# Kernel optimization log

Measured on AMD Instinct MI355X. Metric: run time of the kernel, lower is better.

Reference implementation:

```python
import jax, jax.numpy as jnp
import numpy as np

D_MODEL = 1024
D_HIDDEN = 4096
BATCH = 4
SEQ = 2048
EPS = 1e-5
SLOPE = 0.01  # LeakyReLU default negative_slope


def layer_norm(x, g, b):
    m = jnp.mean(x, axis=-1, keepdims=True)
    v = jnp.mean(jnp.square(x - m), axis=-1, keepdims=True)
    return (x - m) * jax.lax.rsqrt(v + EPS) * g + b


def leaky_relu(x):
    return jnp.where(x >= 0, x, SLOPE * x)


def setup_inputs() -> dict:
    key = jax.random.key(0)
    ks = jax.random.split(key, 8)
    scale = D_MODEL ** 0.5
    x = jax.random.normal(ks[0], (BATCH, SEQ, D_MODEL), dtype=jnp.float32)
    qk = jax.random.normal(ks[1], (D_MODEL, D_MODEL), dtype=jnp.float32) / scale
    ov = jax.random.normal(ks[2], (D_MODEL, D_MODEL), dtype=jnp.float32) / scale
    ln1_g = jnp.ones((D_MODEL,), jnp.float32)
    ln1_b = jnp.zeros((D_MODEL,), jnp.float32)
    ln2_g = jnp.ones((D_MODEL,), jnp.float32)
    ln2_b = jnp.zeros((D_MODEL,), jnp.float32)
    # nn.Linear default init: uniform(-1/sqrt(fan_in), 1/sqrt(fan_in))
    def lin(k, fan_in, fan_out):
        k1, k2 = jax.random.split(k)
        bd = 1.0 / np.sqrt(fan_in)
        W = jax.random.uniform(k1, (fan_out, fan_in), jnp.float32, -bd, bd)
        b = jax.random.uniform(k2, (fan_out,), jnp.float32, -bd, bd)
        return W, b
    W_up, b_up = lin(ks[3], D_MODEL, D_HIDDEN)
    W_h, b_h = lin(ks[4], D_HIDDEN, D_HIDDEN)
    W_down, b_down = lin(ks[5], D_HIDDEN, D_MODEL)
    return {"x": x, "qk": qk, "ov": ov, "ln1_g": ln1_g, "ln1_b": ln1_b,
            "ln2_g": ln2_g, "ln2_b": ln2_b, "W_up": W_up, "b_up": b_up,
            "W_h": W_h, "b_h": b_h, "W_down": W_down, "b_down": b_down}


def reference(x, qk, ov, ln1_g, ln1_b, ln2_g, ln2_b,
              W_up, b_up, W_h, b_h, W_down, b_down):
    scale = D_MODEL ** 0.5
    # --- attention on ln1(x) ---
    h = layer_norm(x, ln1_g, ln1_b)                     # [B,S,D]
    scores = jnp.einsum('bsd,de,bte->bst', h, qk, h) / scale  # [B,S,S]
    n = h.shape[1]
    causal = jnp.tril(jnp.ones((n, n), bool))
    scores = jnp.where(causal, scores, -jnp.inf)
    probs = jax.nn.softmax(scores, axis=-1)
    attn = jnp.einsum('bst,btd,de->bse', probs, h, ov)  # [B,S,D]
    x = x + attn
    # --- MLP on ln2(x) ---
    h2 = layer_norm(x, ln2_g, ln2_b)
    a = leaky_relu(h2 @ W_up.T + b_up)
    a = leaky_relu(a @ W_h.T + b_h)
    a = leaky_relu(a @ W_down.T + b_down)
    return x + a
```

## Files before the change

kernel.cpp:

```cpp
#include <hip/hip_runtime.h>
#include <stdint.h>


typedef __attribute__((ext_vector_type(4))) float  f32x4;
typedef __attribute__((ext_vector_type(8))) __bf16 bf16v8;
typedef __attribute__((ext_vector_type(8))) unsigned short u16x8;
typedef unsigned short ushort_t;
typedef unsigned int   u32;

#define SLOPE 0.01f

__device__ __forceinline__ ushort_t f2bf(float f) {
  u32 u = __builtin_bit_cast(u32, f);
  u32 r = (u + 0x7FFFu + ((u >> 16) & 1u)) >> 16;
  return (ushort_t)r;
}
__device__ __forceinline__ float bf2f(ushort_t b) {
  u32 u = ((u32)b) << 16;
  return __builtin_bit_cast(float, u);
}

__device__ __forceinline__ void gload_lds16(const void* g, void* l) {
  __builtin_amdgcn_global_load_lds(
      (const __attribute__((address_space(1))) u32*)g,
      (__attribute__((address_space(3))) u32*)l, 16, 0, 0);
}

template<int EPI>
__global__ __launch_bounds__(512, 1)
void gemm_nt8(const ushort_t* __restrict__ A, const ushort_t* __restrict__ B,
              void* __restrict__ Cv, const float* __restrict__ bias,
              int M, int N, int K)
{
  extern __shared__ char smem[];
  const ushort_t* lds = (const ushort_t*)smem;
  const int tid = threadIdx.x;
  const int l   = tid & 63;
  const int m0 = blockIdx.y * 256;
  const int n0 = blockIdx.x * 256;
  const int wid = tid >> 6;
  const int wm = (wid >> 2) * 128;
  const int wn = (wid & 3) * 64;
  const int nt = K >> 5;

  const int  sg      = (((tid & 3) ^ ((tid >> 3) & 3))) * 8;
  const long rowA0   = (long)(m0 +       (tid >> 2)) * K;
  const long rowA1   = (long)(m0 + 128 + (tid >> 2)) * K;
  const long rowB0   = (long)(n0 +       (tid >> 2)) * K;
  const long rowB1   = (long)(n0 + 128 + (tid >> 2)) * K;
  const int  wbase16 = (tid & ~63) * 16;

#define STAGE(TT) do {                                                        \
    const long _k  = (long)(TT) * 32;                                         \
    char* _ra = (char*)smem + ((TT) & 3) * 32768 + wbase16;                   \
    char* _rb = _ra + 16384;                                                  \
    gload_lds16(A + rowA0 + _k + sg, _ra);                                    \
    gload_lds16(A + rowA1 + _k + sg, _ra + 8192);                             \
    gload_lds16(B + rowB0 + _k + sg, _rb);                                    \
    gload_lds16(B + rowB1 + _k + sg, _rb + 8192);                             \
  } while (0)

  const int fr  = l & 15;
  const int fsl = (((l >> 4) ^ ((l >> 1) & 3))) * 8;

  f32x4 acc[8][4] = {};

  STAGE(0);
  if (nt > 1) STAGE(1);
  if (nt > 2) STAGE(2);
  if (nt > 2)      { asm volatile("s_waitcnt vmcnt(8)" ::: "memory"); }
  else if (nt > 1) { asm volatile("s_waitcnt vmcnt(4)" ::: "memory"); }
  else             { asm volatile("s_waitcnt vmcnt(0)" ::: "memory"); }
  __builtin_amdgcn_s_barrier();
  __builtin_amdgcn_sched_barrier(0);

  for (int t = 0; t < nt; ++t) {
    const int buf = t & 3;
    const ushort_t* rA = lds + buf * 16384 +        (wm + fr) * 32 + fsl;
    const ushort_t* rB = lds + buf * 16384 + 8192 + (wn + fr) * 32 + fsl;
    bf16v8 av[8], bv[4];
#pragma unroll
    for (int mf = 0; mf < 8; mf++) av[mf] = *(const bf16v8*)(rA + mf * 512);
#pragma unroll
    for (int nf = 0; nf < 4; nf++) bv[nf] = *(const bf16v8*)(rB + nf * 512);

    if (t + 3 < nt) STAGE(t + 3);

    __builtin_amdgcn_s_setprio(1);
#pragma unroll
    for (int mf = 0; mf < 8; mf++)
#pragma unroll
      for (int nf = 0; nf < 4; nf++)
        acc[mf][nf] = __builtin_amdgcn_mfma_f32_16x16x32_bf16(
            av[mf], bv[nf], acc[mf][nf], 0, 0, 0);
    __builtin_amdgcn_s_setprio(0);

    if (t <= nt - 4) {
      asm volatile("s_waitcnt vmcnt(8)" ::: "memory");
      __builtin_amdgcn_s_barrier();
      __builtin_amdgcn_sched_barrier(0);
    } else if (t == nt - 3) {
      asm volatile("s_waitcnt vmcnt(4)" ::: "memory");
      __builtin_amdgcn_s_barrier();
      __builtin_amdgcn_sched_barrier(0);
    } else if (t == nt - 2) {
      asm volatile("s_waitcnt vmcnt(0)" ::: "memory");
      __builtin_amdgcn_s_barrier();
      __builtin_amdgcn_sched_barrier(0);
    }
  }
#undef STAGE

  const int lr = (l >> 4) * 4;
#pragma unroll
  for (int mf = 0; mf < 8; mf++) {
    const int row0 = m0 + wm + mf * 16 + lr;
#pragma unroll
    for (int nf = 0; nf < 4; nf++) {
      const int col = n0 + wn + nf * 16 + fr;
      const float bcol = bias ? bias[col] : 0.f;
#pragma unroll
      for (int r = 0; r < 4; r++) {
        float v = acc[mf][nf][r];
        if constexpr (EPI == 2) {
          v += bcol;
          v = v >= 0.f ? v : SLOPE * v;
          ((ushort_t*)Cv)[(long)(row0 + r) * N + col] = f2bf(v);
        } else {
          ((ushort_t*)Cv)[(long)(row0 + r) * N + col] = f2bf(v);
        }
      }
    }
  }
}

template<int EPI, bool CAUSAL, bool KLIM>
__global__ __launch_bounds__(256)
void gemm_nt(const ushort_t* __restrict__ A, const ushort_t* __restrict__ B,
             void* __restrict__ Cv, const float* __restrict__ bias,
             const float* __restrict__ resid,
             int M, int N, int K, long sAb, long sBb, long sCb)
{
  __shared__ ushort_t lA[128 * 32];
  __shared__ ushort_t lB[128 * 32];
  const int tid = threadIdx.x;
  const int w = tid >> 6;
  const int l = tid & 63;
  const int m0 = blockIdx.y * 128;
  const int n0 = blockIdx.x * 128;
  if (CAUSAL && n0 > m0 + 127) return;
  const long bz = blockIdx.z;
  A += bz * sAb;
  B += bz * sBb;
  int Keff = K;
  if (KLIM) Keff = min(K, m0 + 128);

  const ushort_t* gA = A + (long)(m0 + w * 32 + (l >> 2)) * K + (l & 3) * 8;
  const ushort_t* gB = B + (long)(n0 + w * 32 + (l >> 2)) * K + (l & 3) * 8;
  ushort_t* lAw0 = &lA[(w * 32) * 32];
  ushort_t* lAw1 = &lA[(w * 32 + 16) * 32];
  ushort_t* lBw0 = &lB[(w * 32) * 32];
  ushort_t* lBw1 = &lB[(w * 32 + 16) * 32];
  const int wm = (w >> 1) * 64, wn = (w & 1) * 64;

  f32x4 acc[4][4] = {};

  for (int k0 = 0; k0 < Keff; k0 += 32) {
    gload_lds16(gA,                 lAw0);
    gload_lds16(gA + (long)16 * K,  lAw1);
    gload_lds16(gB,                 lBw0);
    gload_lds16(gB + (long)16 * K,  lBw1);
    gA += 32; gB += 32;
    __syncthreads();

    bf16v8 af[4], bfr[4];
#pragma unroll
    for (int m = 0; m < 4; m++)
      af[m] = *(const bf16v8*)&lA[(wm + m * 16 + (l & 15)) * 32 + (l >> 4) * 8];
#pragma unroll
    for (int n = 0; n < 4; n++)
      bfr[n] = *(const bf16v8*)&lB[(wn + n * 16 + (l & 15)) * 32 + (l >> 4) * 8];
#pragma unroll
    for (int m = 0; m < 4; m++)
#pragma unroll
      for (int n = 0; n < 4; n++)
        acc[m][n] = __builtin_amdgcn_mfma_f32_16x16x32_bf16(af[m], bfr[n], acc[m][n], 0, 0, 0);
    __syncthreads();
  }

  const int lr = (l >> 4) * 4;
  const int lc = l & 15;
#pragma unroll
  for (int m = 0; m < 4; m++) {
    const int row0 = m0 + wm + m * 16 + lr;
#pragma unroll
    for (int n = 0; n < 4; n++) {
      const int col = n0 + wn + n * 16 + lc;
#pragma unroll
      for (int r = 0; r < 4; r++) {
        float v = acc[m][n][r];
        const long idx = bz * sCb + (long)(row0 + r) * N + col;
        if constexpr (EPI == 0) {
          ((ushort_t*)Cv)[idx] = f2bf(v);
        } else if constexpr (EPI == 2) {
          v += bias[col];
          v = v >= 0.f ? v : SLOPE * v;
          ((ushort_t*)Cv)[idx] = f2bf(v);
        } else if constexpr (EPI == 3) {
          ((float*)Cv)[idx] = v + resid[idx];
        } else {
          v += bias[col];
          v = v >= 0.f ? v : SLOPE * v;
          ((float*)Cv)[idx] = v + resid[idx];
        }
      }
    }
  }
}

__global__ __launch_bounds__(256)
void ln_kernel(const float* __restrict__ x, const float* __restrict__ g,
               const float* __restrict__ bta, ushort_t* __restrict__ o)
{
  const long row = blockIdx.x;
  const int tid = threadIdx.x;
  const float4 v = *((const float4*)(x + row * 1024) + tid);
  float s  = v.x + v.y + v.z + v.w;
  float ss = v.x * v.x + v.y * v.y + v.z * v.z + v.w * v.w;
  for (int o2 = 32; o2 > 0; o2 >>= 1) {
    s  += __shfl_down(s, o2);
    ss += __shfl_down(ss, o2);
  }
  __shared__ float rs[4], rss[4];
  const int w = tid >> 6, l = tid & 63;
  if (l == 0) { rs[w] = s; rss[w] = ss; }
  __syncthreads();
  if (tid == 0) {
    float a = 0, c = 0;
    for (int i = 0; i < 4; i++) { a += rs[i]; c += rss[i]; }
    rs[0] = a; rss[0] = c;
  }
  __syncthreads();
  const float mean = rs[0] * (1.f / 1024.f);
  const float var  = rss[0] * (1.f / 1024.f) - mean * mean;
  const float rstd = rsqrtf(var + 1e-5f);
  const int c0 = tid * 4;
  ushort_t* orow = o + row * 1024;
  const float* vp = (const float*)&v;
#pragma unroll
  for (int i = 0; i < 4; i++)
    orow[c0 + i] = f2bf((vp[i] - mean) * rstd * g[c0 + i] + bta[c0 + i]);
}

__global__ __launch_bounds__(256)
void softmax_kernel(ushort_t* __restrict__ sc)
{
  const long row = blockIdx.x;
  const int s = (int)(row & 2047);
  const int tid = threadIdx.x;
  ushort_t* srow = sc + row * 2048;
  const int t0 = tid * 8;
  u16x8 raw = *(const u16x8*)(srow + t0);
  float v[8];
  const float rsc = 1.0f / 32.0f;
  float mx = -3e38f;
#pragma unroll
  for (int i = 0; i < 8; i++) {
    float f = bf2f(raw[i]) * rsc;
    v[i] = (t0 + i <= s) ? f : -3e38f;
    mx = fmaxf(mx, v[i]);
  }
  for (int o = 32; o > 0; o >>= 1) mx = fmaxf(mx, __shfl_down(mx, o));
  __shared__ float red[8];
  const int w = tid >> 6, l = tid & 63;
  if (l == 0) red[w] = mx;
  __syncthreads();
  if (tid == 0) {
    float m2 = red[0];
    for (int i = 1; i < 4; i++) m2 = fmaxf(m2, red[i]);
    red[0] = m2;
  }
  __syncthreads();
  const float m = red[0];
  float sum = 0.f;
#pragma unroll
  for (int i = 0; i < 8; i++) {
    float e = (t0 + i <= s) ? __expf(v[i] - m) : 0.f;
    v[i] = e; sum += e;
  }
  for (int o = 32; o > 0; o >>= 1) sum += __shfl_down(sum, o);
  if (l == 0) red[4 + w] = sum;
  __syncthreads();
  if (tid == 0) {
    float s2 = 0;
    for (int i = 0; i < 4; i++) s2 += red[4 + i];
    red[0] = 1.0f / s2;
  }
  __syncthreads();
  const float inv = red[0];
#pragma unroll
  for (int i = 0; i < 8; i++) srow[t0 + i] = f2bf(v[i] * inv);
}

__global__ __launch_bounds__(256)
void cast3_bf16(const float* __restrict__ a, const float* __restrict__ b,
                const float* __restrict__ c, ushort_t* __restrict__ oa,
                ushort_t* __restrict__ ob, ushort_t* __restrict__ oc)
{
  long i = ((long)blockIdx.x * 256 + threadIdx.x) * 4;
  const float* src; ushort_t* dst;
  if (i < 4194304L)        { src = a; dst = oa; }
  else if (i < 8388608L)   { src = b + (0 - 4194304L); dst = ob - 4194304L; }
  else                     { src = c + (0 - 8388608L); dst = oc - 8388608L; }
  float4 v = *(const float4*)(src + i);
  dst[i]     = f2bf(v.x);
  dst[i + 1] = f2bf(v.y);
  dst[i + 2] = f2bf(v.z);
  dst[i + 3] = f2bf(v.w);
}

__global__ __launch_bounds__(256)
void transpose_cast2(const float* __restrict__ s0, ushort_t* __restrict__ d0,
                     const float* __restrict__ s1, ushort_t* __restrict__ d1)
{
  __shared__ ushort_t t[32][33];
  const float* in = blockIdx.z ? s1 : s0;
  ushort_t*    o  = blockIdx.z ? d1 : d0;
  const int tx = threadIdx.x & 31, ty = threadIdx.x >> 5;
  const int r0 = blockIdx.y * 32, c0 = blockIdx.x * 32;
#pragma unroll
  for (int i = 0; i < 4; i++)
    t[ty + i * 8][tx] = f2bf(in[(long)(r0 + ty + i * 8) * 1024 + c0 + tx]);
  __syncthreads();
#pragma unroll
  for (int i = 0; i < 4; i++)
    o[(long)(c0 + ty + i * 8) * 1024 + r0 + tx] = t[tx][ty + i * 8];
}

__global__ __launch_bounds__(256)
void transpose_bf16(const ushort_t* __restrict__ in, ushort_t* __restrict__ o,
                    int R, int C)
{
  __shared__ ushort_t t[32][33];
  const long bz = blockIdx.z;
  in += bz * (long)R * C;
  o  += bz * (long)R * C;
  const int tx = threadIdx.x & 31, ty = threadIdx.x >> 5;
  const int r0 = blockIdx.y * 32, c0 = blockIdx.x * 32;
#pragma unroll
  for (int i = 0; i < 4; i++)
    t[ty + i * 8][tx] = in[(long)(r0 + ty + i * 8) * C + c0 + tx];
  __syncthreads();
#pragma unroll
  for (int i = 0; i < 4; i++)
    o[(long)(c0 + ty + i * 8) * R + r0 + tx] = t[tx][ty + i * 8];
}

extern "C" void kernel_launch(void* const* d_in, const int* in_sizes, int n_in,
                              void* d_out, int out_size, void* d_ws, size_t ws_size,
                              hipStream_t stream)
{
  const float* x      = (const float*)d_in[0];
  const float* qk     = (const float*)d_in[1];
  const float* ov     = (const float*)d_in[2];
  const float* ln1_g  = (const float*)d_in[3];
  const float* ln1_b  = (const float*)d_in[4];
  const float* ln2_g  = (const float*)d_in[5];
  const float* ln2_b  = (const float*)d_in[6];
  const float* W_up   = (const float*)d_in[7];
  const float* b_up   = (const float*)d_in[8];
  const float* W_h    = (const float*)d_in[9];
  const float* b_h    = (const float*)d_in[10];
  const float* W_down = (const float*)d_in[11];
  const float* b_down = (const float*)d_in[12];
  float* out = (float*)d_out;
  char* ws = (char*)d_ws;
  const long MB = 1024L * 1024L;

  ushort_t* wqT    = (ushort_t*)(ws +   0 * MB);
  ushort_t* woT    = (ushort_t*)(ws +   2 * MB);
  ushort_t* h      = (ushort_t*)(ws +   4 * MB);
  ushort_t* hT     = (ushort_t*)(ws +  20 * MB);
  ushort_t* q      = (ushort_t*)(ws +  36 * MB);
  ushort_t* scores = (ushort_t*)(ws +  52 * MB);
  ushort_t* h2     = h;
  ushort_t* attnh  = q;
  ushort_t* wu     = hT;
  ushort_t* wd     = (ushort_t*)(ws +  28 * MB);
  ushort_t* wh     = q;
  ushort_t* a1c    = (ushort_t*)(ws +  68 * MB);
  ushort_t* a2     = (ushort_t*)(ws + 100 * MB);

  const bool bigws = ws_size >= (size_t)(166 * MB);

  transpose_cast2<<<dim3(32, 32, 2), 256, 0, stream>>>(qk, wqT, ov, woT);
  ln_kernel<<<8192, 256, 0, stream>>>(x, ln1_g, ln1_b, h);
  transpose_bf16<<<dim3(32, 64, 4), 256, 0, stream>>>(h, hT, 2048, 1024);

  gemm_nt<0, false, false><<<dim3(8, 64, 1), 256, 0, stream>>>(
      h, wqT, q, nullptr, nullptr, 8192, 1024, 1024, 0, 0, 0);
  gemm_nt<0, true, false><<<dim3(16, 16, 4), 256, 0, stream>>>(
      q, h, scores, nullptr, nullptr, 2048, 2048, 1024,
      2048L * 1024, 2048L * 1024, 2048L * 2048);
  softmax_kernel<<<8192, 256, 0, stream>>>(scores);
  gemm_nt<0, false, true><<<dim3(8, 16, 4), 256, 0, stream>>>(
      scores, hT, attnh, nullptr, nullptr, 2048, 1024, 2048,
      2048L * 2048, 1024L * 2048, 2048L * 1024);
  gemm_nt<3, false, false><<<dim3(8, 64, 1), 256, 0, stream>>>(
      attnh, woT, out, nullptr, x, 8192, 1024, 1024, 0, 0, 0);

  ln_kernel<<<8192, 256, 0, stream>>>(out, ln2_g, ln2_b, h2);
  cast3_bf16<<<24576, 256, 0, stream>>>(W_up, W_down, W_h, wu, wd, wh);

  if (bigws) {
    for (int c = 0; c < 2; c++) {
      const long r0 = (long)c * 4096;
      gemm_nt8<2><<<dim3(16, 16, 1), 512, 131072, stream>>>(
          h2 + r0 * 1024, wu, a1c, b_up, 4096, 4096, 1024);
      gemm_nt8<2><<<dim3(16, 16, 1), 512, 131072, stream>>>(
          a1c, wh, a2 + r0 * 4096, b_h, 4096, 4096, 4096);
    }
    gemm_nt<4, false, false><<<dim3(8, 64, 1), 256, 0, stream>>>(
        a2, wd, out, b_down, out, 8192, 1024, 4096, 0, 0, 0);
  } else {
    for (int c = 0; c < 2; c++) {
      const long r0 = (long)c * 4096;
      gemm_nt8<2><<<dim3(16, 16, 1), 512, 131072, stream>>>(
          h2 + r0 * 1024, wu, a1c, b_up, 4096, 4096, 1024);
      gemm_nt8<2><<<dim3(16, 16, 1), 512, 131072, stream>>>(
          a1c, wh, a2, b_h, 4096, 4096, 4096);
      gemm_nt<4, false, false><<<dim3(8, 32, 1), 256, 0, stream>>>(
          a2, wd, out + r0 * 1024, b_down, out + r0 * 1024, 4096, 1024, 4096, 0, 0, 0);
    }
  }
}
```

Before: 685.0 us.

## Split GEMM K-tiles into half-phase ping-pong schedule and remap blocks per XCD

The 256x256 GEMM main loop is restructured into two half-tile phases. A and B staging is split, the next tile's fragments are prefetched into double-buffered registers, and extra barriers interleave LDS reads, global loads and MFMA bursts. Both GEMM kernels also remap workgroup IDs so consecutive logical tiles land on the same XCD, which should improve L2 reuse. The schedule adds barriers and register pressure, and it assumes an even K-tile count because the loop steps by two.

```diff
diff --git a/kernel.cpp b/kernel.cpp
--- a/kernel.cpp
+++ b/kernel.cpp
@@ -36,8 +36,13 @@
   const ushort_t* lds = (const ushort_t*)smem;
   const int tid = threadIdx.x;
   const int l   = tid & 63;
-  const int m0 = blockIdx.y * 256;
-  const int n0 = blockIdx.x * 256;
+  const int nwg = gridDim.x * gridDim.y;
+  const int orig = blockIdx.y * gridDim.x + blockIdx.x;
+  const int q8 = nwg >> 3, r8 = nwg & 7;
+  const int xcd = orig & 7, io = orig >> 3;
+  const int logical = (xcd < r8 ? xcd * (q8 + 1) : r8 * (q8 + 1) + (xcd - r8) * q8) + io;
+  const int m0 = (logical / gridDim.x) * 256;
+  const int n0 = (logical % gridDim.x) * 256;
   const int wid = tid >> 6;
   const int wm = (wid >> 2) * 128;
   const int wn = (wid & 3) * 64;
@@ -50,12 +55,15 @@
   const long rowB1   = (long)(n0 + 128 + (tid >> 2)) * K;
   const int  wbase16 = (tid & ~63) * 16;
 
-#define STAGE(TT) do {                                                        \
+#define STAGE_A(TT) do {                                                      \
     const long _k  = (long)(TT) * 32;                                         \
     char* _ra = (char*)smem + ((TT) & 3) * 32768 + wbase16;                   \
-    char* _rb = _ra + 16384;                                                  \
     gload_lds16(A + rowA0 + _k + sg, _ra);                                    \
     gload_lds16(A + rowA1 + _k + sg, _ra + 8192);                             \
+  } while (0)
+#define STAGE_B(TT) do {                                                      \
+    const long _k  = (long)(TT) * 32;                                         \
+    char* _rb = (char*)smem + ((TT) & 3) * 32768 + 16384 + wbase16;           \
     gload_lds16(B + rowB0 + _k + sg, _rb);                                    \
     gload_lds16(B + rowB1 + _k + sg, _rb + 8192);                             \
   } while (0)
@@ -64,52 +72,74 @@
   const int fsl = (((l >> 4) ^ ((l >> 1) & 3))) * 8;
 
   f32x4 acc[8][4] = {};
-
-  STAGE(0);
-  if (nt > 1) STAGE(1);
-  if (nt > 2) STAGE(2);
-  if (nt > 2)      { asm volatile("s_waitcnt vmcnt(8)" ::: "memory"); }
-  else if (nt > 1) { asm volatile("s_waitcnt vmcnt(4)" ::: "memory"); }
-  else             { asm volatile("s_waitcnt vmcnt(0)" ::: "memory"); }
+  bf16v8 avL0[4], bv0[4], avL1[4], bv1[4], avH[4];
+
+  STAGE_A(0); STAGE_B(0);
+  STAGE_A(1); STAGE_B(1);
+  STAGE_A(2); STAGE_B(2);
+  asm volatile("s_waitcnt vmcnt(8)" ::: "memory");
   __builtin_amdgcn_s_barrier();
   __builtin_amdgcn_sched_barrier(0);
-
-  for (int t = 0; t < nt; ++t) {
-    const int buf = t & 3;
-    const ushort_t* rA = lds + buf * 16384 +        (wm + fr) * 32 + fsl;
-    const ushort_t* rB = lds + buf * 16384 + 8192 + (wn + fr) * 32 + fsl;
-    bf16v8 av[8], bv[4];
-#pragma unroll
-    for (int mf = 0; mf < 8; mf++) av[mf] = *(const bf16v8*)(rA + mf * 512);
-#pragma unroll
-    for (int nf = 0; nf < 4; nf++) bv[nf] = *(const bf16v8*)(rB + nf * 512);
-
-    if (t + 3 < nt) STAGE(t + 3);
-
-    __builtin_amdgcn_s_setprio(1);
-#pragma unroll
-    for (int mf = 0; mf < 8; mf++)
-#pragma unroll
-      for (int nf = 0; nf < 4; nf++)
-        acc[mf][nf] = __builtin_amdgcn_mfma_f32_16x16x32_bf16(
-            av[mf], bv[nf], acc[mf][nf], 0, 0, 0);
-    __builtin_amdgcn_s_setprio(0);
-
-    if (t <= nt - 4) {
-      asm volatile("s_waitcnt vmcnt(8)" ::: "memory");
-      __builtin_amdgcn_s_barrier();
-      __builtin_amdgcn_sched_barrier(0);
-    } else if (t == nt - 3) {
-      asm volatile("s_waitcnt vmcnt(4)" ::: "memory");
-      __builtin_amdgcn_s_barrier();
-      __builtin_amdgcn_sched_barrier(0);
-    } else if (t == nt - 2) {
-      asm volatile("s_waitcnt vmcnt(0)" ::: "memory");
-      __builtin_amdgcn_s_barrier();
-      __builtin_amdgcn_sched_barrier(0);
-    }
-  }
-#undef STAGE
+  {
+    const ushort_t* rA = lds +        (wm + fr) * 32 + fsl;
+    const ushort_t* rB = lds + 8192 + (wn + fr) * 32 + fsl;
+#pragma unroll
+    for (int j = 0; j < 4; j++) bv0[j]  = *(const bf16v8*)(rB + j * 512);
+#pragma unroll
+    for (int j = 0; j < 4; j++) avL0[j] = *(const bf16v8*)(rA + j * 512);
+  }
+
+#define TILE(T, avL, bvv, avLn, bvn) do {                                     \
+    const int _buf = (T) & 3;                                                 \
+    const ushort_t* _rA = lds + _buf * 16384 +        (wm + fr) * 32 + fsl;   \
+                                                  \
+    _Pragma("unroll")                                                         \
+    for (int j = 0; j < 4; j++) avH[j] = *(const bf16v8*)(_rA + (j + 4) * 512);\
+    if ((T) + 3 < nt) STAGE_A((T) + 3);                                       \
+    __builtin_amdgcn_s_barrier();                                             \
+    __builtin_amdgcn_s_setprio(1);                                            \
+    _Pragma("unroll")                                                         \
+    for (int mf = 0; mf < 4; mf++)                                            \
+      _Pragma("unroll")                                                       \
+      for (int nf = 0; nf < 4; nf++)                                          \
+        acc[mf][nf] = __builtin_amdgcn_mfma_f32_16x16x32_bf16(                \
+            avL[mf], bvv[nf], acc[mf][nf], 0, 0, 0);                          \
+    __builtin_amdgcn_s_setprio(0);                                            \
+    if ((T) + 3 < nt)      { asm volatile("s_waitcnt vmcnt(6)" ::: "memory"); }\
+    else if ((T) + 2 < nt) { asm volatile("s_waitcnt vmcnt(4)" ::: "memory"); }\
+    else                   { asm volatile("s_waitcnt vmcnt(0)" ::: "memory"); }\
+    __builtin_amdgcn_s_barrier();                                             \
+    __builtin_amdgcn_sched_barrier(0);                                        \
+                                                  \
+    if ((T) + 1 < nt) {                                                       \
+      const int _bufn = ((T) + 1) & 3;                                        \
+      const ushort_t* _rAn = lds + _bufn * 16384 +        (wm + fr) * 32 + fsl;\
+      const ushort_t* _rBn = lds + _bufn * 16384 + 8192 + (wn + fr) * 32 + fsl;\
+      _Pragma("unroll")                                                       \
+      for (int j = 0; j < 4; j++) bvn[j]  = *(const bf16v8*)(_rBn + j * 512); \
+      _Pragma("unroll")                                                       \
+      for (int j = 0; j < 4; j++) avLn[j] = *(const bf16v8*)(_rAn + j * 512); \
+    }                                                                         \
+    if ((T) + 3 < nt) STAGE_B((T) + 3);                                       \
+    __builtin_amdgcn_s_barrier();                                             \
+    __builtin_amdgcn_s_setprio(1);                                            \
+    _Pragma("unroll")                                                         \
+    for (int mf = 0; mf < 4; mf++)                                            \
+      _Pragma("unroll")                                                       \
+      for (int nf = 0; nf < 4; nf++)                                          \
+        acc[mf + 4][nf] = __builtin_amdgcn_mfma_f32_16x16x32_bf16(            \
+            avH[mf], bvv[nf], acc[mf + 4][nf], 0, 0, 0);                      \
+    __builtin_amdgcn_s_setprio(0);                                            \
+    __builtin_amdgcn_s_barrier();                                             \
+  } while (0)
+
+  for (int t = 0; t < nt; t += 2) {
+    TILE(t,     avL0, bv0, avL1, bv1);
+    TILE(t + 1, avL1, bv1, avL0, bv0);
+  }
+#undef TILE
+#undef STAGE_A
+#undef STAGE_B
 
   const int lr = (l >> 4) * 4;
 #pragma unroll
@@ -146,8 +176,13 @@
   const int tid = threadIdx.x;
   const int w = tid >> 6;
   const int l = tid & 63;
-  const int m0 = blockIdx.y * 128;
-  const int n0 = blockIdx.x * 128;
+  const int nwg = gridDim.x * gridDim.y;
+  const int orig = blockIdx.y * gridDim.x + blockIdx.x;
+  const int q8 = nwg >> 3, r8 = nwg & 7;
+  const int xcd = orig & 7, io = orig >> 3;
+  const int logical = (xcd < r8 ? xcd * (q8 + 1) : r8 * (q8 + 1) + (xcd - r8) * q8) + io;
+  const int m0 = (logical / gridDim.x) * 128;
+  const int n0 = (logical % gridDim.x) * 128;
   if (CAUSAL && n0 > m0 + 127) return;
   const long bz = blockIdx.z;
   A += bz * sAb;
```

After: 691.0 us. Within noise of the previous version (+0.9%).
